# Kernel optimization log

Measured on AMD Instinct MI355X. Metric: run time of the kernel, lower is better.

Reference implementation:

```python
import jax, jax.numpy as jnp
import numpy as np

S, B, C = 7, 2, 80
LAMBDA_COORDS = 5.0
LAMBDA_NOOBJ = 0.5


def _iou_cxcywh(a, b):
    """Elementwise IoU of boxes in cx,cy,w,h format, shapes (..., 4) -> (...).
    Same math as torchvision box_convert(cxcywh->xyxy) + box_iou diagonal,
    computed directly (O(S^2)) instead of the O(S^4) pairwise matrix."""
    ax1 = a[..., 0] - a[..., 2] * 0.5
    ay1 = a[..., 1] - a[..., 3] * 0.5
    ax2 = a[..., 0] + a[..., 2] * 0.5
    ay2 = a[..., 1] + a[..., 3] * 0.5
    bx1 = b[..., 0] - b[..., 2] * 0.5
    by1 = b[..., 1] - b[..., 3] * 0.5
    bx2 = b[..., 0] + b[..., 2] * 0.5
    by2 = b[..., 1] + b[..., 3] * 0.5
    inter_w = jnp.clip(jnp.minimum(ax2, bx2) - jnp.maximum(ax1, bx1), 0.0)
    inter_h = jnp.clip(jnp.minimum(ay2, by2) - jnp.maximum(ay1, by1), 0.0)
    inter = inter_w * inter_h
    area_a = (ax2 - ax1) * (ay2 - ay1)
    area_b = (bx2 - bx1) * (by2 - by1)
    return inter / (area_a + area_b - inter)


def setup_inputs() -> dict:
    key = jax.random.key(0)
    k1, k2 = jax.random.split(key)
    N = 8192
    predictions = jax.random.normal(k1, (N, S, S, C + 5 * B), dtype=jnp.float32)
    target = jax.random.uniform(k2, (N, S, S, C + 5), dtype=jnp.float32)
    return {"predictions": predictions, "target": target}


def reference(predictions, target):
    preds = predictions.reshape(-1, S, S, C + 5 * B)
    target_boxes = target[..., -4:]                 # (N,S,S,4)
    pred_boxes_1 = preds[..., -4:]
    pred_boxes_2 = preds[..., -9:-5]

    iou1 = _iou_cxcywh(pred_boxes_1, target_boxes)  # (N,S,S) == diag of box_iou
    iou2 = _iou_cxcywh(pred_boxes_2, target_boxes)
    ious_idx = jnp.argmax(jnp.stack([iou1, iou2], axis=0), axis=0)  # (N,S,S)

    m1 = (1 - ious_idx).astype(preds.dtype)  # responsible-box masks
    m2 = ious_idx.astype(preds.dtype)
    obj = target[..., -5]                    # objectness (N,S,S)

    pred_boxes = obj[..., None] * (m1[..., None] * pred_boxes_1 + m2[..., None] * pred_boxes_2)

    dims = jnp.sign(pred_boxes[..., -2:]) * jnp.sqrt(jnp.abs(pred_boxes[..., -2:]) + 1e-6)
    target_dims = jnp.sqrt(target_boxes[..., -2:])

    sse = lambda a, b: jnp.sum((a - b) ** 2)  # MSELoss(reduction='sum')

    center_loss = sse(pred_boxes[..., :-3], target_boxes[..., :-3]) * LAMBDA_COORDS
    dimensions_loss = sse(dims, target_dims) * LAMBDA_COORDS
    coords_loss = center_loss + dimensions_loss

    obj_pred = preds[..., -5] * m1 + preds[..., -10] * m2
    obj_loss = sse(obj * obj_pred, obj)
    noobj_loss = sse((1.0 - obj) * obj_pred, obj) * LAMBDA_NOOBJ

    classes_loss = sse(preds[..., :-10] * obj[..., None], target[..., :-5])

    return (coords_loss, obj_loss, noobj_loss, classes_loss)
```

## Files before the change

kernel.cpp:

```cpp
#include <hip/hip_runtime.h>


#define NPRED 90
#define NTGT  85
#define NCLS  80
#define BLOCK 256

__device__ __forceinline__ float sgnf(float x) {
    return (x > 0.0f) ? 1.0f : ((x < 0.0f) ? -1.0f : 0.0f);
}

struct CellLoads { float p0, p1, t0, t1; };

__device__ __forceinline__ void process_cell(
    const CellLoads& L, int lane,
    float& coords, float& objl, float& noobjl, float& clsl)
{
    float obj = __shfl(L.t1, 16);

    float d0 = fmaf(L.p0, obj, -L.t0);
    float acc = d0 * d0;
    if (lane < 16) {
        float d1 = fmaf(L.p1, obj, -L.t1);
        acc = fmaf(d1, d1, acc);
    }
    clsl += acc;

    float P80 = __shfl(L.p1, 16), P81 = __shfl(L.p1, 17);
    float P82 = __shfl(L.p1, 18), P83 = __shfl(L.p1, 19);
    float P84 = __shfl(L.p1, 20), P85 = __shfl(L.p1, 21);
    float P86 = __shfl(L.p1, 22);
    float P88 = __shfl(L.p1, 24), P89 = __shfl(L.p1, 25);
    float P87 = __shfl(L.p1, 23);
    float tcx = __shfl(L.t1, 17), tcy = __shfl(L.t1, 18);
    float tw  = __shfl(L.t1, 19), th  = __shfl(L.t1, 20);

    if (lane == 0) {
        float bx1 = tcx - tw * 0.5f, by1 = tcy - th * 0.5f;
        float bx2 = tcx + tw * 0.5f, by2 = tcy + th * 0.5f;
        float area_b = (bx2 - bx1) * (by2 - by1);

        float ax1 = P86 - P88 * 0.5f, ay1 = P87 - P89 * 0.5f;
        float ax2 = P86 + P88 * 0.5f, ay2 = P87 + P89 * 0.5f;
        float iw = fmaxf(fminf(ax2, bx2) - fmaxf(ax1, bx1), 0.0f);
        float ih = fmaxf(fminf(ay2, by2) - fmaxf(ay1, by1), 0.0f);
        float inter1 = iw * ih;
        float area1 = (ax2 - ax1) * (ay2 - ay1);
        float iou1 = inter1 / (area1 + area_b - inter1);

        float cx1 = P81 - P83 * 0.5f, cy1 = P82 - P84 * 0.5f;
        float cx2 = P81 + P83 * 0.5f, cy2 = P82 + P84 * 0.5f;
        float jw = fmaxf(fminf(cx2, bx2) - fmaxf(cx1, bx1), 0.0f);
        float jh = fmaxf(fminf(cy2, by2) - fmaxf(cy1, by1), 0.0f);
        float inter2 = jw * jh;
        float area2 = (cx2 - cx1) * (cy2 - cy1);
        float iou2 = inter2 / (area2 + area_b - inter2);

        bool use2 = iou2 > iou1;

        float pcx = obj * (use2 ? P81 : P86);
        float pw  = obj * (use2 ? P83 : P88);
        float ph  = obj * (use2 ? P84 : P89);

        float dc = pcx - tcx;
        float dw = sgnf(pw) * sqrtf(fabsf(pw) + 1e-6f) - sqrtf(tw);
        float dh = sgnf(ph) * sqrtf(fabsf(ph) + 1e-6f) - sqrtf(th);
        coords = fmaf(dc, dc, coords);
        coords = fmaf(dw, dw, coords);
        coords = fmaf(dh, dh, coords);

        float obj_pred = use2 ? P80 : P85;
        float e1 = fmaf(obj, obj_pred, -obj);
        objl = fmaf(e1, e1, objl);
        float e2 = fmaf(1.0f - obj, obj_pred, -obj);
        noobjl = fmaf(e2, e2, noobjl);
    }
}

__device__ __forceinline__ CellLoads load_cell(
    const float* __restrict__ preds, const float* __restrict__ targ,
    int c, int lane)
{
    const float* p = preds + (size_t)c * NPRED;
    const float* t = targ  + (size_t)c * NTGT;
    CellLoads L;
    L.p0 = p[lane];
    L.p1 = (lane < NPRED - 64) ? p[64 + lane] : 0.0f;
    L.t0 = t[lane];
    L.t1 = (lane < NTGT - 64) ? t[64 + lane] : 0.0f;
    return L;
}

__global__ __launch_bounds__(BLOCK) void yolo_loss_kernel(
    const float* __restrict__ preds, const float* __restrict__ targ,
    float* __restrict__ out, int n_cells)
{
    const int lane = threadIdx.x & 63;
    const int gw   = blockIdx.x * (BLOCK / 64) + (threadIdx.x >> 6);
    const int W    = gridDim.x * (BLOCK / 64);

    float coords = 0.0f, objl = 0.0f, noobjl = 0.0f, clsl = 0.0f;

    int c = gw * 2;
    for (; c + 1 < n_cells; c += 2 * W) {
        CellLoads A = load_cell(preds, targ, c, lane);
        CellLoads B = load_cell(preds, targ, c + 1, lane);
        process_cell(A, lane, coords, objl, noobjl, clsl);
        process_cell(B, lane, coords, objl, noobjl, clsl);
    }
    if (c < n_cells) {
        CellLoads A = load_cell(preds, targ, c, lane);
        process_cell(A, lane, coords, objl, noobjl, clsl);
    }

    #pragma unroll
    for (int off = 32; off > 0; off >>= 1) {
        coords += __shfl_down(coords, off);
        objl   += __shfl_down(objl, off);
        noobjl += __shfl_down(noobjl, off);
        clsl   += __shfl_down(clsl, off);
    }

    __shared__ float red[4][4];
    int wave = threadIdx.x >> 6;
    if (lane == 0) {
        red[0][wave] = coords;
        red[1][wave] = objl;
        red[2][wave] = noobjl;
        red[3][wave] = clsl;
    }
    __syncthreads();
    if (threadIdx.x == 0) {
        float cd = red[0][0] + red[0][1] + red[0][2] + red[0][3];
        float o  = red[1][0] + red[1][1] + red[1][2] + red[1][3];
        float n  = red[2][0] + red[2][1] + red[2][2] + red[2][3];
        float k  = red[3][0] + red[3][1] + red[3][2] + red[3][3];
        atomicAdd(&out[0], 5.0f * cd);
        atomicAdd(&out[1], o);
        atomicAdd(&out[2], 0.5f * n);
        atomicAdd(&out[3], k);
    }
}

extern "C" void kernel_launch(void* const* d_in, const int* in_sizes, int n_in,
                              void* d_out, int out_size, void* d_ws, size_t ws_size,
                              hipStream_t stream) {
    const float* preds = (const float*)d_in[0];
    const float* targ  = (const float*)d_in[1];
    float* out = (float*)d_out;

    int n_cells = in_sizes[0] / NPRED;

    hipMemsetAsync(d_out, 0, (size_t)out_size * sizeof(float), stream);

    int blocks = 2048;
    hipLaunchKernelGGL(yolo_loss_kernel, dim3(blocks), dim3(BLOCK), 0, stream,
                       preds, targ, out, n_cells);
}
```

Baseline: 369.2 us.

## Stream 64-cell tiles with flat coalesced loads and per-thread box math

Replaces the one-wave-per-cell scheme, which issued partial 90/85-float row loads and many cross-lane shuffles, with a block-wide tile of 64 cells. The block reads the tile's contiguous prediction range in a flat loop, computes the class SSE inline, and stages box and objectness fields in shared memory. One thread per cell then does the IoU and coordinate math, removing the shuffles and the single-lane serial work. The cost is a divide by 90 per element, gathered target loads, three barriers per tile, and bank-strided shared-memory writes.

```diff
diff --git a/kernel.cpp b/kernel.cpp
--- a/kernel.cpp
+++ b/kernel.cpp
@@ -4,113 +4,102 @@
 #define NPRED 90
 #define NTGT  85
 #define NCLS  80
+#define TILE  64
 #define BLOCK 256
 
 __device__ __forceinline__ float sgnf(float x) {
     return (x > 0.0f) ? 1.0f : ((x < 0.0f) ? -1.0f : 0.0f);
 }
 
-struct CellLoads { float p0, p1, t0, t1; };
-
-__device__ __forceinline__ void process_cell(
-    const CellLoads& L, int lane,
-    float& coords, float& objl, float& noobjl, float& clsl)
-{
-    float obj = __shfl(L.t1, 16);
-
-    float d0 = fmaf(L.p0, obj, -L.t0);
-    float acc = d0 * d0;
-    if (lane < 16) {
-        float d1 = fmaf(L.p1, obj, -L.t1);
-        acc = fmaf(d1, d1, acc);
-    }
-    clsl += acc;
-
-    float P80 = __shfl(L.p1, 16), P81 = __shfl(L.p1, 17);
-    float P82 = __shfl(L.p1, 18), P83 = __shfl(L.p1, 19);
-    float P84 = __shfl(L.p1, 20), P85 = __shfl(L.p1, 21);
-    float P86 = __shfl(L.p1, 22);
-    float P88 = __shfl(L.p1, 24), P89 = __shfl(L.p1, 25);
-    float P87 = __shfl(L.p1, 23);
-    float tcx = __shfl(L.t1, 17), tcy = __shfl(L.t1, 18);
-    float tw  = __shfl(L.t1, 19), th  = __shfl(L.t1, 20);
-
-    if (lane == 0) {
-        float bx1 = tcx - tw * 0.5f, by1 = tcy - th * 0.5f;
-        float bx2 = tcx + tw * 0.5f, by2 = tcy + th * 0.5f;
-        float area_b = (bx2 - bx1) * (by2 - by1);
-
-        float ax1 = P86 - P88 * 0.5f, ay1 = P87 - P89 * 0.5f;
-        float ax2 = P86 + P88 * 0.5f, ay2 = P87 + P89 * 0.5f;
-        float iw = fmaxf(fminf(ax2, bx2) - fmaxf(ax1, bx1), 0.0f);
-        float ih = fmaxf(fminf(ay2, by2) - fmaxf(ay1, by1), 0.0f);
-        float inter1 = iw * ih;
-        float area1 = (ax2 - ax1) * (ay2 - ay1);
-        float iou1 = inter1 / (area1 + area_b - inter1);
-
-        float cx1 = P81 - P83 * 0.5f, cy1 = P82 - P84 * 0.5f;
-        float cx2 = P81 + P83 * 0.5f, cy2 = P82 + P84 * 0.5f;
-        float jw = fmaxf(fminf(cx2, bx2) - fmaxf(cx1, bx1), 0.0f);
-        float jh = fmaxf(fminf(cy2, by2) - fmaxf(cy1, by1), 0.0f);
-        float inter2 = jw * jh;
-        float area2 = (cx2 - cx1) * (cy2 - cy1);
-        float iou2 = inter2 / (area2 + area_b - inter2);
-
-        bool use2 = iou2 > iou1;
-
-        float pcx = obj * (use2 ? P81 : P86);
-        float pw  = obj * (use2 ? P83 : P88);
-        float ph  = obj * (use2 ? P84 : P89);
-
-        float dc = pcx - tcx;
-        float dw = sgnf(pw) * sqrtf(fabsf(pw) + 1e-6f) - sqrtf(tw);
-        float dh = sgnf(ph) * sqrtf(fabsf(ph) + 1e-6f) - sqrtf(th);
-        coords = fmaf(dc, dc, coords);
-        coords = fmaf(dw, dw, coords);
-        coords = fmaf(dh, dh, coords);
-
-        float obj_pred = use2 ? P80 : P85;
-        float e1 = fmaf(obj, obj_pred, -obj);
-        objl = fmaf(e1, e1, objl);
-        float e2 = fmaf(1.0f - obj, obj_pred, -obj);
-        noobjl = fmaf(e2, e2, noobjl);
-    }
-}
-
-__device__ __forceinline__ CellLoads load_cell(
-    const float* __restrict__ preds, const float* __restrict__ targ,
-    int c, int lane)
-{
-    const float* p = preds + (size_t)c * NPRED;
-    const float* t = targ  + (size_t)c * NTGT;
-    CellLoads L;
-    L.p0 = p[lane];
-    L.p1 = (lane < NPRED - 64) ? p[64 + lane] : 0.0f;
-    L.t0 = t[lane];
-    L.t1 = (lane < NTGT - 64) ? t[64 + lane] : 0.0f;
-    return L;
-}
-
 __global__ __launch_bounds__(BLOCK) void yolo_loss_kernel(
     const float* __restrict__ preds, const float* __restrict__ targ,
-    float* __restrict__ out, int n_cells)
+    float* __restrict__ out, int n_cells, int n_tiles)
 {
-    const int lane = threadIdx.x & 63;
-    const int gw   = blockIdx.x * (BLOCK / 64) + (threadIdx.x >> 6);
-    const int W    = gridDim.x * (BLOCK / 64);
+    __shared__ float s_obj[TILE];
+    __shared__ float s_pbox[TILE * 11];
+    __shared__ float s_tbox[TILE * 5];
+    __shared__ float red[4][4];
 
+    const int tid = threadIdx.x;
     float coords = 0.0f, objl = 0.0f, noobjl = 0.0f, clsl = 0.0f;
 
-    int c = gw * 2;
-    for (; c + 1 < n_cells; c += 2 * W) {
-        CellLoads A = load_cell(preds, targ, c, lane);
-        CellLoads B = load_cell(preds, targ, c + 1, lane);
-        process_cell(A, lane, coords, objl, noobjl, clsl);
-        process_cell(B, lane, coords, objl, noobjl, clsl);
-    }
-    if (c < n_cells) {
-        CellLoads A = load_cell(preds, targ, c, lane);
-        process_cell(A, lane, coords, objl, noobjl, clsl);
+    for (int tile = blockIdx.x; tile < n_tiles; tile += gridDim.x) {
+        int cell0 = tile * TILE;
+        int ncell = min(TILE, n_cells - cell0);
+        const float* pb = preds + (size_t)cell0 * NPRED;
+        const float* tb = targ  + (size_t)cell0 * NTGT;
+
+        __syncthreads();
+        if (tid < ncell) s_obj[tid] = tb[tid * NTGT + NCLS];
+        __syncthreads();
+
+        int nelem = ncell * NPRED;
+        for (int j = tid; j < nelem; j += BLOCK) {
+            unsigned cell = (unsigned)j / 90u;
+            int field = j - (int)cell * 90;
+            float p = pb[j];
+            if (field < 85) {
+                float tv = tb[(int)cell * 85 + field];
+                if (field < 80) {
+                    float d = fmaf(p, s_obj[cell], -tv);
+                    clsl = fmaf(d, d, clsl);
+                } else {
+                    if (field >= 81) s_tbox[cell * 5 + (field - 81)] = tv;
+                    s_pbox[cell * 11 + (field - 80)] = p;
+                }
+            } else {
+                s_pbox[cell * 11 + (field - 80)] = p;
+            }
+        }
+        __syncthreads();
+
+        if (tid < ncell) {
+            const float* pc = s_pbox + tid * 11;
+            float obj = s_obj[tid];
+            float P80 = pc[0], P81 = pc[1], P82 = pc[2], P83 = pc[3], P84 = pc[4];
+            float P85 = pc[5], P86 = pc[6], P87 = pc[7], P88 = pc[8], P89 = pc[9];
+            float tcx = s_tbox[tid * 5 + 0], tcy = s_tbox[tid * 5 + 1];
+            float tw  = s_tbox[tid * 5 + 2], th  = s_tbox[tid * 5 + 3];
+
+            float bx1 = tcx - tw * 0.5f, by1 = tcy - th * 0.5f;
+            float bx2 = tcx + tw * 0.5f, by2 = tcy + th * 0.5f;
+            float area_b = (bx2 - bx1) * (by2 - by1);
+
+            float ax1 = P86 - P88 * 0.5f, ay1 = P87 - P89 * 0.5f;
+            float ax2 = P86 + P88 * 0.5f, ay2 = P87 + P89 * 0.5f;
+            float iw = fmaxf(fminf(ax2, bx2) - fmaxf(ax1, bx1), 0.0f);
+            float ih = fmaxf(fminf(ay2, by2) - fmaxf(ay1, by1), 0.0f);
+            float inter1 = iw * ih;
+            float area1 = (ax2 - ax1) * (ay2 - ay1);
+            float iou1 = inter1 / (area1 + area_b - inter1);
+
+            float cx1 = P81 - P83 * 0.5f, cy1 = P82 - P84 * 0.5f;
+            float cx2 = P81 + P83 * 0.5f, cy2 = P82 + P84 * 0.5f;
+            float jw = fmaxf(fminf(cx2, bx2) - fmaxf(cx1, bx1), 0.0f);
+            float jh = fmaxf(fminf(cy2, by2) - fmaxf(cy1, by1), 0.0f);
+            float inter2 = jw * jh;
+            float area2 = (cx2 - cx1) * (cy2 - cy1);
+            float iou2 = inter2 / (area2 + area_b - inter2);
+
+            bool use2 = iou2 > iou1;
+
+            float pcx = obj * (use2 ? P81 : P86);
+            float pw  = obj * (use2 ? P83 : P88);
+            float ph  = obj * (use2 ? P84 : P89);
+
+            float dc = pcx - tcx;
+            float dw = sgnf(pw) * sqrtf(fabsf(pw) + 1e-6f) - sqrtf(tw);
+            float dh = sgnf(ph) * sqrtf(fabsf(ph) + 1e-6f) - sqrtf(th);
+            coords = fmaf(dc, dc, coords);
+            coords = fmaf(dw, dw, coords);
+            coords = fmaf(dh, dh, coords);
+
+            float obj_pred = use2 ? P80 : P85;
+            float e1 = fmaf(obj, obj_pred, -obj);
+            objl = fmaf(e1, e1, objl);
+            float e2 = fmaf(1.0f - obj, obj_pred, -obj);
+            noobjl = fmaf(e2, e2, noobjl);
+        }
     }
 
     #pragma unroll
@@ -121,8 +110,9 @@
         clsl   += __shfl_down(clsl, off);
     }
 
-    __shared__ float red[4][4];
-    int wave = threadIdx.x >> 6;
+    int wave = tid >> 6;
+    int lane = tid & 63;
+    __syncthreads();
     if (lane == 0) {
         red[0][wave] = coords;
         red[1][wave] = objl;
@@ -130,7 +120,7 @@
         red[3][wave] = clsl;
     }
     __syncthreads();
-    if (threadIdx.x == 0) {
+    if (tid == 0) {
         float cd = red[0][0] + red[0][1] + red[0][2] + red[0][3];
         float o  = red[1][0] + red[1][1] + red[1][2] + red[1][3];
         float n  = red[2][0] + red[2][1] + red[2][2] + red[2][3];
@@ -150,10 +140,12 @@
     float* out = (float*)d_out;
 
     int n_cells = in_sizes[0] / NPRED;
+    int n_tiles = (n_cells + TILE - 1) / TILE;
 
     hipMemsetAsync(d_out, 0, (size_t)out_size * sizeof(float), stream);
 
     int blocks = 2048;
+    if (blocks > n_tiles) blocks = n_tiles;
     hipLaunchKernelGGL(yolo_loss_kernel, dim3(blocks), dim3(BLOCK), 0, stream,
-                       preds, targ, out, n_cells);
+                       preds, targ, out, n_cells, n_tiles);
 }
```

Result: slower. 412.1 us (+11.6%).

## Split class loss into flat elementwise pass and per-thread box pass

Applied to the files above, without the earlier changes.

Replaces the one-wave-per-cell mapping with two phases. The first is a flat grid-stride loop over all prediction elements that computes the class SSE, using a divide by 90 to recover the cell and field. The second is a per-thread-per-cell loop that loads the box fields with float2 vector loads and computes the IoU, coordinate and objectness terms. The aim is to remove the cross-lane shuffles and the lane-0 serialization where most lanes sat idle. In exchange it adds integer division per element, re-reads obj per element, and makes the box pass use strided, uncoalesced accesses that touch the tail cache lines a second time.

```diff
diff --git a/kernel.cpp b/kernel.cpp
--- a/kernel.cpp
+++ b/kernel.cpp
@@ -10,32 +10,50 @@
     return (x > 0.0f) ? 1.0f : ((x < 0.0f) ? -1.0f : 0.0f);
 }
 
-struct CellLoads { float p0, p1, t0, t1; };
+__device__ __forceinline__ void class_elem(
+    const float* __restrict__ preds, const float* __restrict__ targ,
+    int j, float& clsl)
+{
+    unsigned cell = (unsigned)j / 90u;
+    int field = j - (int)cell * 90;
+    if (field < NCLS) {
+        float p   = preds[j];
+        float tv  = targ[(int)cell * NTGT + field];
+        float obj = targ[(int)cell * NTGT + NCLS];
+        float d = fmaf(p, obj, -tv);
+        clsl = fmaf(d, d, clsl);
+    }
+}
 
-__device__ __forceinline__ void process_cell(
-    const CellLoads& L, int lane,
-    float& coords, float& objl, float& noobjl, float& clsl)
+__global__ __launch_bounds__(BLOCK) void yolo_loss_kernel(
+    const float* __restrict__ preds, const float* __restrict__ targ,
+    float* __restrict__ out, int n_cells)
 {
-    float obj = __shfl(L.t1, 16);
+    const int gtid = blockIdx.x * BLOCK + threadIdx.x;
+    const int T    = gridDim.x * BLOCK;
 
-    float d0 = fmaf(L.p0, obj, -L.t0);
-    float acc = d0 * d0;
-    if (lane < 16) {
-        float d1 = fmaf(L.p1, obj, -L.t1);
-        acc = fmaf(d1, d1, acc);
+    float coords = 0.0f, objl = 0.0f, noobjl = 0.0f, clsl = 0.0f;
+
+    const int N = n_cells * NPRED;
+    int j = gtid;
+    for (; j + 3 * T < N; j += 4 * T) {
+        class_elem(preds, targ, j,         clsl);
+        class_elem(preds, targ, j + T,     clsl);
+        class_elem(preds, targ, j + 2 * T, clsl);
+        class_elem(preds, targ, j + 3 * T, clsl);
     }
-    clsl += acc;
+    for (; j < N; j += T) class_elem(preds, targ, j, clsl);
 
-    float P80 = __shfl(L.p1, 16), P81 = __shfl(L.p1, 17);
-    float P82 = __shfl(L.p1, 18), P83 = __shfl(L.p1, 19);
-    float P84 = __shfl(L.p1, 20), P85 = __shfl(L.p1, 21);
-    float P86 = __shfl(L.p1, 22);
-    float P88 = __shfl(L.p1, 24), P89 = __shfl(L.p1, 25);
-    float P87 = __shfl(L.p1, 23);
-    float tcx = __shfl(L.t1, 17), tcy = __shfl(L.t1, 18);
-    float tw  = __shfl(L.t1, 19), th  = __shfl(L.t1, 20);
+    for (int c = gtid; c < n_cells; c += T) {
+        const float* p = preds + (size_t)c * NPRED;
+        const float* t = targ  + (size_t)c * NTGT;
+        const float2* pb = (const float2*)(p + 80);
+        float2 q0 = pb[0], q1 = pb[1], q2 = pb[2], q3 = pb[3], q4 = pb[4];
+        float P80 = q0.x, P81 = q0.y, P82 = q1.x, P83 = q1.y, P84 = q2.x;
+        float P85 = q2.y, P86 = q3.x, P87 = q3.y, P88 = q4.x, P89 = q4.y;
+        float obj = t[80];
+        float tcx = t[81], tcy = t[82], tw = t[83], th = t[84];
 
-    if (lane == 0) {
         float bx1 = tcx - tw * 0.5f, by1 = tcy - th * 0.5f;
         float bx2 = tcx + tw * 0.5f, by2 = tcy + th * 0.5f;
         float area_b = (bx2 - bx1) * (by2 - by1);
@@ -75,43 +93,6 @@
         float e2 = fmaf(1.0f - obj, obj_pred, -obj);
         noobjl = fmaf(e2, e2, noobjl);
     }
-}
-
-__device__ __forceinline__ CellLoads load_cell(
-    const float* __restrict__ preds, const float* __restrict__ targ,
-    int c, int lane)
-{
-    const float* p = preds + (size_t)c * NPRED;
-    const float* t = targ  + (size_t)c * NTGT;
-    CellLoads L;
-    L.p0 = p[lane];
-    L.p1 = (lane < NPRED - 64) ? p[64 + lane] : 0.0f;
-    L.t0 = t[lane];
-    L.t1 = (lane < NTGT - 64) ? t[64 + lane] : 0.0f;
-    return L;
-}
-
-__global__ __launch_bounds__(BLOCK) void yolo_loss_kernel(
-    const float* __restrict__ preds, const float* __restrict__ targ,
-    float* __restrict__ out, int n_cells)
-{
-    const int lane = threadIdx.x & 63;
-    const int gw   = blockIdx.x * (BLOCK / 64) + (threadIdx.x >> 6);
-    const int W    = gridDim.x * (BLOCK / 64);
-
-    float coords = 0.0f, objl = 0.0f, noobjl = 0.0f, clsl = 0.0f;
-
-    int c = gw * 2;
-    for (; c + 1 < n_cells; c += 2 * W) {
-        CellLoads A = load_cell(preds, targ, c, lane);
-        CellLoads B = load_cell(preds, targ, c + 1, lane);
-        process_cell(A, lane, coords, objl, noobjl, clsl);
-        process_cell(B, lane, coords, objl, noobjl, clsl);
-    }
-    if (c < n_cells) {
-        CellLoads A = load_cell(preds, targ, c, lane);
-        process_cell(A, lane, coords, objl, noobjl, clsl);
-    }
 
     #pragma unroll
     for (int off = 32; off > 0; off >>= 1) {
@@ -123,6 +104,7 @@
 
     __shared__ float red[4][4];
     int wave = threadIdx.x >> 6;
+    int lane = threadIdx.x & 63;
     if (lane == 0) {
         red[0][wave] = coords;
         red[1][wave] = objl;
```

After: 384.3 us. +4.1%, slower.
